# Kernel tuning notes

Measured on AMD Instinct MI355X. Metric: run time of the kernel, lower is better.

Reference implementation:

```python
import jax, jax.numpy as jnp
import numpy as np

T, B, IC = 512, 64, 512
HC, L = 512, 2

def setup_inputs() -> dict:
    key = jax.random.key(0)
    ks = jax.random.split(key, 4)
    # xavier_normal-ish scale for weights
    s1 = (2.0 / (IC + HC + 2 * HC)) ** 0.5
    s2 = (2.0 / (IC + HC + HC)) ** 0.5
    return {
        "x": jax.random.normal(ks[0], (T, B, IC), dtype=jnp.float32),
        "hiddens": jax.random.normal(ks[1], (L, 1, HC), dtype=jnp.float32),
        "W1": jax.random.normal(ks[2], (L, 2 * HC, IC + HC), dtype=jnp.float32) * s1,
        "b1": jnp.ones((L, 2 * HC), dtype=jnp.float32),
        "W2": jax.random.normal(ks[3], (L, HC, IC + HC), dtype=jnp.float32) * s2,
        "b2": jnp.zeros((L, HC), dtype=jnp.float32),
    }

def _gru_layer(xs, h0, W1l, b1l, W2l, b2l):
    # xs: [T, B, ic], h0: [B, hc]
    def step(h, xt):
        pre = jnp.concatenate([xt, h], axis=1) @ W1l.T + b1l  # [B, 2*hc]
        r = jax.nn.sigmoid(pre[:, :HC])
        z = jax.nn.sigmoid(pre[:, HC:])
        g = jnp.tanh(jnp.concatenate([xt, r * h], axis=1) @ W2l.T + b2l)
        h_new = z * h + (1.0 - z) * g
        return h_new, h_new
    h_last, hs = jax.lax.scan(step, h0, xs)
    return hs, h_last  # hs: [T, B, hc]

def reference(x, hiddens, W1, b1, W2, b2):
    bs = x.shape[1]
    h0 = jnp.broadcast_to(hiddens, (L, bs, HC))  # repeat over batch
    layer_in = x
    finals = []
    for i in range(L):
        layer_in, h_last = _gru_layer(layer_in, h0[i], W1[i], b1[i], W2[i], b2[i])
        finals.append(h_last)
    out = layer_in                      # [T, B, hc]
    hs = jnp.stack(finals, axis=0)      # [L, B, hc]
    return (out, hs)
```

## Files before the change

### kernel.cpp

```cpp
#include <hip/hip_runtime.h>
#include <hip/hip_bf16.h>


#define T_STEPS 512
#define BATCH   64
#define ICH     512
#define HCH     512
#define NL      2
#define M_TOT   (T_STEPS*BATCH)
#define N1      (2*HCH)
#define KCAT    (ICH+HCH)
#define NWG     64
#define NTHR    512

using bf16x8  = __attribute__((ext_vector_type(8))) __bf16;
using floatx4 = __attribute__((ext_vector_type(4))) float;
using uint4v  = __attribute__((ext_vector_type(4))) unsigned int;

__device__ __forceinline__ unsigned short f2bf(float f) {
    unsigned int u = __builtin_bit_cast(unsigned int, f);
    u += 0x7FFFu + ((u >> 16) & 1u);
    return (unsigned short)(u >> 16);
}
__device__ __forceinline__ float bf2f(unsigned short s) {
    unsigned int u = ((unsigned int)s) << 16;
    return __builtin_bit_cast(float, u);
}
__device__ __forceinline__ float sigmoidf_(float x) {
    return 1.0f / (1.0f + __expf(-x));
}
__device__ __forceinline__ floatx4 mfma_bf16(bf16x8 a, bf16x8 b, floatx4 c) {
    return __builtin_amdgcn_mfma_f32_16x16x32_bf16(a, b, c, 0, 0, 0);
}

__device__ __forceinline__ bf16x8 ld_frag_co(const unsigned short* p) {
    union { unsigned long long q[2]; bf16x8 v; } u;
    u.q[0] = __hip_atomic_load((const unsigned long long*)p,
                               __ATOMIC_RELAXED, __HIP_MEMORY_SCOPE_AGENT);
    u.q[1] = __hip_atomic_load(((const unsigned long long*)p) + 1,
                               __ATOMIC_RELAXED, __HIP_MEMORY_SCOPE_AGENT);
    return u.v;
}
__device__ __forceinline__ void st_word_co(unsigned short* p, unsigned int w) {
    __hip_atomic_store((unsigned int*)p, w, __ATOMIC_RELAXED, __HIP_MEMORY_SCOPE_AGENT);
}

__global__ void prep_kernel(const float* __restrict__ x,
                            const float* __restrict__ W1,
                            const float* __restrict__ W2,
                            unsigned short* __restrict__ xb,
                            unsigned short* __restrict__ W1b,
                            unsigned short* __restrict__ W2b) {
    const int NX  = M_TOT*ICH;
    const int NW1 = NL*N1*KCAT;
    const int NW2 = NL*HCH*KCAT;
    const int total = NX + NW1 + NW2;
    for (int i = blockIdx.x*blockDim.x + threadIdx.x; i < total;
         i += gridDim.x*blockDim.x) {
        if (i < NX)           xb[i]         = f2bf(x[i]);
        else if (i < NX+NW1)  W1b[i-NX]     = f2bf(W1[i-NX]);
        else                  W2b[i-NX-NW1] = f2bf(W2[i-NX-NW1]);
    }
}

#define XP_LDP 40
__global__ void __launch_bounds__(256)
xproj_kernel(int layer,
             const unsigned short* __restrict__ Ab,
             const unsigned short* __restrict__ W1b,
             const unsigned short* __restrict__ W2b,
             const float* __restrict__ b1,
             const float* __restrict__ b2,
             unsigned short* __restrict__ X1p,
             unsigned short* __restrict__ X2p) {
    __shared__ unsigned short Ash[128*XP_LDP];
    __shared__ unsigned short Bsh[128*XP_LDP];
    const int nb = blockIdx.x;
    const int mb = blockIdx.y;
    const int tid = threadIdx.x;
    const int lane = tid & 63;
    const int wv = tid >> 6;
    const int wr = (wv >> 1) * 64;
    const int wc = (wv & 1) * 64;
    const int rfrag = lane & 15;
    const int koff = (lane >> 4) * 8;
    const int n0 = nb * 128;

    floatx4 acc[4][4];
    #pragma unroll
    for (int i=0;i<4;i++)
        #pragma unroll
        for (int j=0;j<4;j++) acc[i][j] = (floatx4)(0.0f);

    for (int kc = 0; kc < ICH/32; ++kc) {
        #pragma unroll
        for (int c = 0; c < 2; ++c) {
            int chunk = tid + c*256;
            int row = chunk >> 2;
            int c8  = (chunk & 3) * 8;
            *reinterpret_cast<uint4v*>(&Ash[row*XP_LDP + c8]) =
                *reinterpret_cast<const uint4v*>(&Ab[(size_t)(mb*128 + row)*ICH + kc*32 + c8]);
            int nrow = n0 + row;
            const unsigned short* bsrc = (nrow < N1)
                ? (W1b + (size_t)(layer*N1 + nrow)*KCAT + kc*32 + c8)
                : (W2b + (size_t)(layer*HCH + (nrow - N1))*KCAT + kc*32 + c8);
            *reinterpret_cast<uint4v*>(&Bsh[row*XP_LDP + c8]) =
                *reinterpret_cast<const uint4v*>(bsrc);
        }
        __syncthreads();
        bf16x8 af[4], bfr[4];
        #pragma unroll
        for (int mt=0; mt<4; ++mt)
            af[mt] = *reinterpret_cast<const bf16x8*>(&Ash[(wr + mt*16 + rfrag)*XP_LDP + koff]);
        #pragma unroll
        for (int nt=0; nt<4; ++nt)
            bfr[nt] = *reinterpret_cast<const bf16x8*>(&Bsh[(wc + nt*16 + rfrag)*XP_LDP + koff]);
        #pragma unroll
        for (int mt=0; mt<4; ++mt)
            #pragma unroll
            for (int nt=0; nt<4; ++nt)
                acc[mt][nt] = mfma_bf16(af[mt], bfr[nt], acc[mt][nt]);
        __syncthreads();
    }

    const int col0 = lane & 15;
    const int row0 = (lane >> 4) * 4;
    #pragma unroll
    for (int mt=0; mt<4; ++mt) {
        #pragma unroll
        for (int nt=0; nt<4; ++nt) {
            int n = n0 + wc + nt*16 + col0;
            #pragma unroll
            for (int r=0; r<4; ++r) {
                int m = mb*128 + wr + mt*16 + row0 + r;
                float v = acc[mt][nt][r];
                if (n < N1) {
                    v += b1[layer*N1 + n];
                    X1p[(size_t)m*N1 + n] = f2bf(v);
                } else {
                    v += b2[layer*HCH + (n - N1)];
                    X2p[(size_t)m*HCH + (n - N1)] = f2bf(v);
                }
            }
        }
    }
}

__device__ __forceinline__ void gbar(unsigned int* cnt, unsigned int* gen,
                                     unsigned int round) {
    __syncthreads();
    if (threadIdx.x == 0) {
        unsigned a = __hip_atomic_fetch_add(cnt, 1u, __ATOMIC_RELAXED,
                                            __HIP_MEMORY_SCOPE_AGENT);
        if (a == round*NWG - 1u) {
            __hip_atomic_store(gen, round, __ATOMIC_RELAXED,
                               __HIP_MEMORY_SCOPE_AGENT);
        } else {
            while (__hip_atomic_load(gen, __ATOMIC_RELAXED,
                                     __HIP_MEMORY_SCOPE_AGENT) < round)
                __builtin_amdgcn_s_sleep(1);
        }
    }
    __syncthreads();
}

__global__ void __launch_bounds__(NTHR, 2)
rec_fused(const unsigned short* __restrict__ X1p,
          const unsigned short* __restrict__ X2p,
          const unsigned short* __restrict__ W1b,
          const unsigned short* __restrict__ W2b,
          const float* __restrict__ b1,
          const float* __restrict__ b2,
          const float* __restrict__ hiddens,
          unsigned short* __restrict__ y0seq,
          unsigned short* __restrict__ h1b,
          unsigned short* __restrict__ rh0,
          unsigned short* __restrict__ rh1,
          float* __restrict__ out,
          float* __restrict__ hs,
          unsigned int* __restrict__ cnt, unsigned int* __restrict__ gen) {
    __shared__ float zsh[BATCH*16];
    const int w     = blockIdx.x;
    const int tid   = threadIdx.x;
    const int lane  = tid & 63;
    const int v     = tid >> 6;
    const int rt    = v & 3;
    const int ct    = v >> 2;
    const int rfrag = lane & 15;
    const int quad  = lane >> 4;
    const int layer = (w >= 32) ? 1 : 0;
    const int c0    = (w & 31) * 16;
    const int arow  = rt*16 + rfrag;
    const int crow  = rt*16 + quad*4;
    const int ccol  = c0 + rfrag;
    const int gcol  = (ct ? HCH : 0) + ccol;

    float hreg[4];
    #pragma unroll
    for (int r=0;r<4;++r) hreg[r] = hiddens[layer*HCH + ccol];
    const float bias1 = b1[(size_t)layer*N1 + gcol];
    const float bias2 = b2[(size_t)layer*HCH + ccol];

    if (ct == 0) {
        unsigned short* dst = layer ? h1b : y0seq;
        #pragma unroll
        for (int r=0;r<4;++r) {
            unsigned short me = f2bf(hreg[r]);
            unsigned ot = (unsigned)__shfl_xor((int)(unsigned)me, 1, 64);
            if (!(lane & 1))
                st_word_co(&dst[(crow+r)*HCH + ccol], (unsigned)me | (ot << 16));
        }
    }
    unsigned rnd = 0;
    gbar(cnt, gen, ++rnd);

    for (int s = 0; s <= T_STEPS; ++s) {
        const int tt     = layer ? (s - 1) : s;
        const int active = layer ? (s >= 1) : (s < T_STEPS);
        const unsigned short* aseq = y0seq + (size_t)s*BATCH*HCH;

        if (active) {
            floatx4 acc = (floatx4)(0.0f);
            const unsigned short* wrow = W1b + ((size_t)layer*N1 + gcol)*KCAT;
            if (!layer) {
                #pragma unroll
                for (int ks=0; ks<16; ++ks) {
                    bf16x8 a = ld_frag_co(&aseq[arow*HCH + ks*32 + quad*8]);
                    bf16x8 b = *reinterpret_cast<const bf16x8*>(&wrow[ICH + ks*32 + quad*8]);
                    acc = mfma_bf16(a, b, acc);
                }
            } else {
                #pragma unroll
                for (int ks=0; ks<16; ++ks) {
                    bf16x8 a = ld_frag_co(&aseq[arow*HCH + ks*32 + quad*8]);
                    bf16x8 b = *reinterpret_cast<const bf16x8*>(&wrow[ks*32 + quad*8]);
                    acc = mfma_bf16(a, b, acc);
                }
                #pragma unroll
                for (int ks=0; ks<16; ++ks) {
                    bf16x8 a = ld_frag_co(&h1b[arow*HCH + ks*32 + quad*8]);
                    bf16x8 b = *reinterpret_cast<const bf16x8*>(&wrow[ICH + ks*32 + quad*8]);
                    acc = mfma_bf16(a, b, acc);
                }
            }
            float pre[4];
            if (!layer) {
                #pragma unroll
                for (int r=0;r<4;++r)
                    pre[r] = acc[r] + bf2f(X1p[(size_t)(tt*BATCH + crow + r)*N1 + gcol]);
            } else {
                #pragma unroll
                for (int r=0;r<4;++r) pre[r] = acc[r] + bias1;
            }
            if (ct == 0) {
                unsigned short* rbuf = layer ? rh1 : rh0;
                #pragma unroll
                for (int r=0;r<4;++r) {
                    float rh = sigmoidf_(pre[r]) * hreg[r];
                    unsigned short me = f2bf(rh);
                    unsigned ot = (unsigned)__shfl_xor((int)(unsigned)me, 1, 64);
                    if (!(lane & 1))
                        st_word_co(&rbuf[(crow+r)*HCH + ccol], (unsigned)me | (ot << 16));
                }
            } else {
                #pragma unroll
                for (int r=0;r<4;++r)
                    zsh[(crow+r)*16 + rfrag] = sigmoidf_(pre[r]);
            }
        }
        gbar(cnt, gen, ++rnd);

        if (active && ct == 0) {
            floatx4 acc = (floatx4)(0.0f);
            const unsigned short* w2row = W2b + ((size_t)layer*HCH + ccol)*KCAT;
            const unsigned short* rbuf = layer ? rh1 : rh0;
            if (!layer) {
                #pragma unroll
                for (int ks=0; ks<16; ++ks) {
                    bf16x8 a = ld_frag_co(&rbuf[arow*HCH + ks*32 + quad*8]);
                    bf16x8 b = *reinterpret_cast<const bf16x8*>(&w2row[ICH + ks*32 + quad*8]);
                    acc = mfma_bf16(a, b, acc);
                }
            } else {
                #pragma unroll
                for (int ks=0; ks<16; ++ks) {
                    bf16x8 a = ld_frag_co(&aseq[arow*HCH + ks*32 + quad*8]);
                    bf16x8 b = *reinterpret_cast<const bf16x8*>(&w2row[ks*32 + quad*8]);
                    acc = mfma_bf16(a, b, acc);
                }
                #pragma unroll
                for (int ks=0; ks<16; ++ks) {
                    bf16x8 a = ld_frag_co(&rbuf[arow*HCH + ks*32 + quad*8]);
                    bf16x8 b = *reinterpret_cast<const bf16x8*>(&w2row[ICH + ks*32 + quad*8]);
                    acc = mfma_bf16(a, b, acc);
                }
            }
            unsigned short* hdst = layer ? h1b
                                         : (y0seq + (size_t)(tt+1)*BATCH*HCH);
            #pragma unroll
            for (int r=0;r<4;++r) {
                float x2 = layer ? bias2
                                 : bf2f(X2p[(size_t)(tt*BATCH + crow + r)*HCH + ccol]);
                float g  = tanhf(acc[r] + x2);
                float z  = zsh[(crow+r)*16 + rfrag];
                float hn = z*hreg[r] + (1.0f - z)*g;
                hreg[r] = hn;
                unsigned short me = f2bf(hn);
                unsigned ot = (unsigned)__shfl_xor((int)(unsigned)me, 1, 64);
                if (!(lane & 1))
                    st_word_co(&hdst[(crow+r)*HCH + ccol], (unsigned)me | (ot << 16));
                if (layer)
                    out[((size_t)tt*BATCH + crow + r)*HCH + ccol] = hn;
                if (tt == T_STEPS-1)
                    hs[(size_t)layer*BATCH*HCH + (crow+r)*HCH + ccol] = hn;
            }
        }
        gbar(cnt, gen, ++rnd);
    }
}

extern "C" void kernel_launch(void* const* d_in, const int* in_sizes, int n_in,
                              void* d_out, int out_size, void* d_ws, size_t ws_size,
                              hipStream_t stream) {
    const float* x       = (const float*)d_in[0];
    const float* hiddens = (const float*)d_in[1];
    const float* W1      = (const float*)d_in[2];
    const float* b1      = (const float*)d_in[3];
    const float* W2      = (const float*)d_in[4];
    const float* b2      = (const float*)d_in[5];
    float* out = (float*)d_out;
    float* hs  = out + (size_t)M_TOT*HCH;

    char* ws = (char*)d_ws;
    size_t off = 0;
    auto alloc = [&](size_t bytes) -> char* {
        char* p = ws + off; off += (bytes + 255) & ~(size_t)255; return p;
    };
    unsigned int*   bar   = (unsigned int*) alloc(1024);
    unsigned short* h1b   = (unsigned short*)alloc((size_t)BATCH*HCH*2);
    unsigned short* rh0   = (unsigned short*)alloc((size_t)BATCH*HCH*2);
    unsigned short* rh1   = (unsigned short*)alloc((size_t)BATCH*HCH*2);
    unsigned short* W1b   = (unsigned short*)alloc((size_t)NL*N1*KCAT*2);
    unsigned short* W2b   = (unsigned short*)alloc((size_t)NL*HCH*KCAT*2);
    unsigned short* xb    = (unsigned short*)alloc((size_t)M_TOT*ICH*2);
    unsigned short* X1p   = (unsigned short*)alloc((size_t)M_TOT*N1*2);
    unsigned short* X2p   = (unsigned short*)alloc((size_t)M_TOT*HCH*2);
    unsigned short* y0seq = (unsigned short*)alloc((size_t)(T_STEPS+1)*BATCH*HCH*2);

    hipMemsetAsync(bar, 0, 1024, stream);
    prep_kernel<<<2048, 256, 0, stream>>>(x, W1, W2, xb, W1b, W2b);
    xproj_kernel<<<dim3(12, 256), 256, 0, stream>>>(0, xb, W1b, W2b, b1, b2, X1p, X2p);
    rec_fused<<<NWG, NTHR, 0, stream>>>(X1p, X2p, W1b, W2b, b1, b2, hiddens,
        y0seq, h1b, rh0, rh1, out, hs, bar, bar + 64);
}
```

Baseline: 18.04 ms.

## Replace atomic-counter grid barrier with per-block flags and layer-aware waits

Replaces the central fetch-add counter barrier with per-workgroup flag slots on padded cache lines. One wavefront polls all 64 flags and waits only on the dependencies each layer needs: layer 0 waits on layer 0 blocks, layer 1 waits on layer 1 and a relaxed round of layer 0. This removes atomic contention on a single counter and the serialized release, and lets the two layers run partly decoupled. Memory ordering relies on relaxed atomics plus coherent stores, so visibility across blocks is a correctness risk.

```diff
diff --git a/kernel.cpp b/kernel.cpp
--- a/kernel.cpp
+++ b/kernel.cpp
@@ -12,6 +12,7 @@
 #define KCAT    (ICH+HCH)
 #define NWG     64
 #define NTHR    512
+#define FLG_STRIDE 8
 
 using bf16x8  = __attribute__((ext_vector_type(8))) __bf16;
 using floatx4 = __attribute__((ext_vector_type(4))) float;
@@ -146,19 +147,21 @@
     }
 }
 
-__device__ __forceinline__ void gbar(unsigned int* cnt, unsigned int* gen,
-                                     unsigned int round) {
+__device__ __forceinline__ void gbar2(unsigned int* flags, unsigned r, int layer) {
     __syncthreads();
-    if (threadIdx.x == 0) {
-        unsigned a = __hip_atomic_fetch_add(cnt, 1u, __ATOMIC_RELAXED,
-                                            __HIP_MEMORY_SCOPE_AGENT);
-        if (a == round*NWG - 1u) {
-            __hip_atomic_store(gen, round, __ATOMIC_RELAXED,
+    if (threadIdx.x < 64) {
+        const unsigned lane = threadIdx.x;
+        if (lane == blockIdx.x)
+            __hip_atomic_store(&flags[lane*FLG_STRIDE], r, __ATOMIC_RELAXED,
                                __HIP_MEMORY_SCOPE_AGENT);
-        } else {
-            while (__hip_atomic_load(gen, __ATOMIC_RELAXED,
-                                     __HIP_MEMORY_SCOPE_AGENT) < round)
-                __builtin_amdgcn_s_sleep(1);
+        const unsigned l0need = (r & 1u) ? r : (r - 1u);
+        const unsigned need = (layer == 0) ? ((lane < 32u) ? r : 0u)
+                                           : ((lane < 32u) ? l0need : r);
+        for (;;) {
+            unsigned v = __hip_atomic_load(&flags[lane*FLG_STRIDE],
+                                           __ATOMIC_RELAXED, __HIP_MEMORY_SCOPE_AGENT);
+            if (__all((int)(v >= need))) break;
+            __builtin_amdgcn_s_sleep(1);
         }
     }
     __syncthreads();
@@ -178,7 +181,7 @@
           unsigned short* __restrict__ rh1,
           float* __restrict__ out,
           float* __restrict__ hs,
-          unsigned int* __restrict__ cnt, unsigned int* __restrict__ gen) {
+          unsigned int* __restrict__ flags) {
     __shared__ float zsh[BATCH*16];
     const int w     = blockIdx.x;
     const int tid   = threadIdx.x;
@@ -212,7 +215,7 @@
         }
     }
     unsigned rnd = 0;
-    gbar(cnt, gen, ++rnd);
+    gbar2(flags, ++rnd, layer);
 
     for (int s = 0; s <= T_STEPS; ++s) {
         const int tt     = layer ? (s - 1) : s;
@@ -268,7 +271,7 @@
                     zsh[(crow+r)*16 + rfrag] = sigmoidf_(pre[r]);
             }
         }
-        gbar(cnt, gen, ++rnd);
+        gbar2(flags, ++rnd, layer);
 
         if (active && ct == 0) {
             floatx4 acc = (floatx4)(0.0f);
@@ -315,7 +318,7 @@
                     hs[(size_t)layer*BATCH*HCH + (crow+r)*HCH + ccol] = hn;
             }
         }
-        gbar(cnt, gen, ++rnd);
+        gbar2(flags, ++rnd, layer);
     }
 }
 
@@ -336,7 +339,7 @@
     auto alloc = [&](size_t bytes) -> char* {
         char* p = ws + off; off += (bytes + 255) & ~(size_t)255; return p;
     };
-    unsigned int*   bar   = (unsigned int*) alloc(1024);
+    unsigned int*   flg   = (unsigned int*) alloc(4096);
     unsigned short* h1b   = (unsigned short*)alloc((size_t)BATCH*HCH*2);
     unsigned short* rh0   = (unsigned short*)alloc((size_t)BATCH*HCH*2);
     unsigned short* rh1   = (unsigned short*)alloc((size_t)BATCH*HCH*2);
@@ -347,9 +350,9 @@
     unsigned short* X2p   = (unsigned short*)alloc((size_t)M_TOT*HCH*2);
     unsigned short* y0seq = (unsigned short*)alloc((size_t)(T_STEPS+1)*BATCH*HCH*2);
 
-    hipMemsetAsync(bar, 0, 1024, stream);
+    hipMemsetAsync(flg, 0, 4096, stream);
     prep_kernel<<<2048, 256, 0, stream>>>(x, W1, W2, xb, W1b, W2b);
     xproj_kernel<<<dim3(12, 256), 256, 0, stream>>>(0, xb, W1b, W2b, b1, b2, X1p, X2p);
     rec_fused<<<NWG, NTHR, 0, stream>>>(X1p, X2p, W1b, W2b, b1, b2, hiddens,
-        y0seq, h1b, rh0, rh1, out, hs, bar, bar + 64);
-}
+        y0seq, h1b, rh0, rh1, out, hs, flg);
+}
```

After: 17.92 ms. About the same (-0.7%).
